# Optimization experiments

Hardware: AMD Instinct MI355X
Metric: run time of the kernel (lower is better)

Reference implementation:

```python
import jax, jax.numpy as jnp
import numpy as np

TEMPERATURE = 8.0  # sqrt(head_dim=64)
NEG_INF = -1e9


def setup_inputs() -> dict:
    key = jax.random.key(0)
    k1, k2, k3, k4, k5 = jax.random.split(key, 5)
    B, H, S, D = 1, 8, 2048, 64
    q = jax.random.normal(k1, (B, H, S, D), dtype=jnp.float32)
    k = jax.random.normal(k2, (B, H, S, D), dtype=jnp.float32)
    v = jax.random.normal(k3, (B, H, S, D), dtype=jnp.float32)
    sph = jax.random.uniform(k4, (B, H, S, S), dtype=jnp.float32)
    mask = jax.random.randint(k5, (B, H, S, S), 0, 2, dtype=jnp.int32)
    return {"q": q, "k": k, "v": v, "sph": sph, "mask": mask}


def reference(q, k, v, sph, mask):
    # scores: [B,H,Sq,Sk]
    attn = jnp.einsum('bhqd,bhkd->bhqk', q / TEMPERATURE, k)
    attn = attn * sph                       # multiplicative bias
    attn = jnp.where(mask == 0, NEG_INF, attn)
    p_attn = jax.nn.softmax(attn, axis=-1)  # dropout p=0 -> identity
    out = jnp.einsum('bhqk,bhkd->bhqd', p_attn, v)
    return (out, p_attn)
```

## Files before the change

### kernel.cpp

```cpp
#include <hip/hip_runtime.h>

#define SLEN 2048
#define DIM  64
#define NH   8
#define TQ   16
#define NEG_INF -1e9f

typedef __attribute__((ext_vector_type(8))) short short8;
typedef __attribute__((ext_vector_type(4))) float f32x4;
typedef unsigned short ushort;

__device__ inline ushort f2bf(float x) {
    unsigned u = __float_as_uint(x);
    u += 0x7fffu + ((u >> 16) & 1u);
    return (ushort)(u >> 16);
}
__device__ inline float bf2f(ushort b) {
    return __uint_as_float(((unsigned)b) << 16);
}

__global__ __launch_bounds__(256)
void convk_kernel(const float* __restrict__ k,
                  ushort* __restrict__ khi, ushort* __restrict__ klo)
{
    int i4 = blockIdx.x * 256 + threadIdx.x;
    float4 x = ((const float4*)k)[i4];
    ushort h0 = f2bf(x.x), h1 = f2bf(x.y), h2 = f2bf(x.z), h3 = f2bf(x.w);
    ushort4 hi = {h0, h1, h2, h3};
    ushort4 lo = {f2bf(x.x - bf2f(h0)), f2bf(x.y - bf2f(h1)),
                  f2bf(x.z - bf2f(h2)), f2bf(x.w - bf2f(h3))};
    ((ushort4*)khi)[i4] = hi;
    ((ushort4*)klo)[i4] = lo;
}

__global__ __launch_bounds__(256)
void convv_kernel(const float* __restrict__ v, ushort* __restrict__ vt)
{
    __shared__ ushort sT[64][70];
    const int h  = blockIdx.x >> 5;
    const int st = blockIdx.x & 31;
    const int t  = threadIdx.x;
    {
        const int r0 = t >> 4;
        const int c  = (t & 15) * 4;
        #pragma unroll
        for (int rr = r0; rr < 64; rr += 16) {
            float4 x = *(const float4*)(v + ((size_t)(h * SLEN + st * 64 + rr)) * DIM + c);
            sT[c + 0][rr] = f2bf(x.x);
            sT[c + 1][rr] = f2bf(x.y);
            sT[c + 2][rr] = f2bf(x.z);
            sT[c + 3][rr] = f2bf(x.w);
        }
    }
    __syncthreads();
    {
        const int d  = t >> 2;
        const int s0 = (t & 3) * 16;
        short8 a = *(const short8*)(&sT[d][s0]);
        short8 b = *(const short8*)(&sT[d][s0 + 8]);
        ushort* dst = vt + ((size_t)(h * DIM + d)) * SLEN + st * 64 + s0;
        *(short8*)(dst)     = a;
        *(short8*)(dst + 8) = b;
    }
}

__global__ __launch_bounds__(256)
void convm_kernel(const int* __restrict__ mask, ushort* __restrict__ mb)
{
    size_t i = (size_t)blockIdx.x * 256 + threadIdx.x;
    const int4* p = (const int4*)(mask + i * 16);
    unsigned m = 0;
    #pragma unroll
    for (int w = 0; w < 4; ++w) {
        int4 a = p[w];
        m |= (a.x != 0 ? 1u : 0u) << (w * 4 + 0);
        m |= (a.y != 0 ? 1u : 0u) << (w * 4 + 1);
        m |= (a.z != 0 ? 1u : 0u) << (w * 4 + 2);
        m |= (a.w != 0 ? 1u : 0u) << (w * 4 + 3);
    }
    mb[i] = (ushort)m;
}

__global__ __launch_bounds__(512, 2)
void attn_mfma_kernel(const float* __restrict__ q,
                      const ushort* __restrict__ khi,
                      const ushort* __restrict__ klo,
                      const ushort* __restrict__ vt,
                      const float* __restrict__ sph,
                      const unsigned* __restrict__ mbits,
                      float* __restrict__ out,
                      float* __restrict__ p_out)
{
    __shared__ ushort sP[TQ][SLEN + 8];
    __shared__ float  sS[TQ][1024 + 4];
    __shared__ ushort sQhi[TQ][72];
    __shared__ ushort sQlo[TQ][72];
    __shared__ float sMax[TQ][8];
    __shared__ float sSum[TQ][8];
    __shared__ float sC[4][TQ][16];

    const int tid  = threadIdx.x;
    const int wave = tid >> 6;
    const int lane = tid & 63;
    const int quad = lane >> 4;
    const int l16  = lane & 15;
    const int bx0  = blockIdx.x;
    const int bx   = ((bx0 & 7) << 7) | (bx0 >> 3);
    const int h    = bx >> 7;
    const int qr0  = (bx & 127) * TQ;

    {
        int e = tid * 2;
        int r = e >> 6, d = e & 63;
        float2 qv = *(const float2*)(q + ((size_t)(h * SLEN + qr0 + r)) * DIM + d);
        ushort h0 = f2bf(qv.x), h1 = f2bf(qv.y);
        sQhi[r][d]     = h0;
        sQhi[r][d + 1] = h1;
        sQlo[r][d]     = f2bf(qv.x - bf2f(h0));
        sQlo[r][d + 1] = f2bf(qv.y - bf2f(h1));
    }
    __syncthreads();

    short8 ah0 = *(const short8*)(&sQhi[l16][quad * 8]);
    short8 ah1 = *(const short8*)(&sQhi[l16][32 + quad * 8]);
    short8 al0 = *(const short8*)(&sQlo[l16][quad * 8]);
    short8 al1 = *(const short8*)(&sQlo[l16][32 + quad * 8]);

    const int cb0 = wave * 128;
    const int cb1 = 1024 + wave * 128;

    unsigned roA[4], roB[4];
    #pragma unroll
    for (int j = 0; j < 4; ++j) {
        unsigned rb = (unsigned)((h * SLEN + qr0 + quad * 4 + j) * SLEN);
        roA[j] = rb + cb0 + l16;
        roB[j] = rb + cb1 + l16;
    }

    unsigned mwA[4][4], mwB[4][4];
    #pragma unroll
    for (int j = 0; j < 4; ++j) {
        const unsigned* mr = mbits
            + (size_t)(h * SLEN + qr0 + quad * 4 + j) * (SLEN / 32);
        *(uint4*)mwA[j] = *(const uint4*)(mr + (cb0 >> 5));
        *(uint4*)mwB[j] = *(const uint4*)(mr + (cb1 >> 5));
    }

    const int srow = wave * 2;
    f32x4 g0[8];
    #pragma unroll
    for (int r = 0; r < 2; ++r)
        #pragma unroll
        for (int i = 0; i < 4; ++i)
            g0[r * 4 + i] = __builtin_nontemporal_load(
                (const f32x4*)(sph + (size_t)(h * SLEN + qr0 + srow + r) * SLEN
                                   + i * 256 + lane * 4));

    f32x4 c[16];
    #pragma unroll
    for (int t = 0; t < 16; ++t) c[t] = (f32x4){0.f, 0.f, 0.f, 0.f};

    #pragma unroll
    for (int t = 0; t < 16; ++t) {
        const int cb = (t < 8) ? (cb0 + t * 16) : (cb1 + (t - 8) * 16);
        const size_t rowb = ((size_t)(h * SLEN + cb + l16)) * DIM + quad * 8;
        short8 bh0 = *(const short8*)(khi + rowb);
        short8 bh1 = *(const short8*)(khi + rowb + 32);
        short8 bl0 = *(const short8*)(klo + rowb);
        short8 bl1 = *(const short8*)(klo + rowb + 32);
        c[t] = __builtin_amdgcn_mfma_f32_16x16x32_bf16(ah0, bh0, c[t], 0, 0, 0);
        c[t] = __builtin_amdgcn_mfma_f32_16x16x32_bf16(ah1, bh1, c[t], 0, 0, 0);
        c[t] = __builtin_amdgcn_mfma_f32_16x16x32_bf16(ah0, bl0, c[t], 0, 0, 0);
        c[t] = __builtin_amdgcn_mfma_f32_16x16x32_bf16(ah1, bl1, c[t], 0, 0, 0);
        c[t] = __builtin_amdgcn_mfma_f32_16x16x32_bf16(al0, bh0, c[t], 0, 0, 0);
        c[t] = __builtin_amdgcn_mfma_f32_16x16x32_bf16(al1, bh1, c[t], 0, 0, 0);
    }

    #pragma unroll
    for (int r = 0; r < 2; ++r)
        #pragma unroll
        for (int i = 0; i < 4; ++i)
            *(f32x4*)&sS[srow + r][i * 256 + lane * 4] = g0[r * 4 + i];
    __syncthreads();

    f32x4 g1[8];
    #pragma unroll
    for (int r = 0; r < 2; ++r)
        #pragma unroll
        for (int i = 0; i < 4; ++i)
            g1[r * 4 + i] = __builtin_nontemporal_load(
                (const f32x4*)(sph + (size_t)(h * SLEN + qr0 + srow + r) * SLEN
                                   + 1024 + i * 256 + lane * 4));

    float rmax[4] = {-3.4e38f, -3.4e38f, -3.4e38f, -3.4e38f};
    #pragma unroll
    for (int t = 0; t < 8; ++t) {
        #pragma unroll
        for (int j = 0; j < 4; ++j) {
            float sphv = sS[quad * 4 + j][cb0 + t * 16 + l16];
            float s = c[t][j] * 0.125f * sphv;
            const unsigned ok = (mwA[j][t >> 1] >> ((t & 1) * 16 + l16)) & 1u;
            s = ok ? s : NEG_INF;
            c[t][j] = s;
            rmax[j] = fmaxf(rmax[j], s);
        }
    }
    __syncthreads();

    #pragma unroll
    for (int r = 0; r < 2; ++r)
        #pragma unroll
        for (int i = 0; i < 4; ++i)
            *(f32x4*)&sS[srow + r][i * 256 + lane * 4] = g1[r * 4 + i];
    __syncthreads();

    #pragma unroll
    for (int t = 8; t < 16; ++t) {
        #pragma unroll
        for (int j = 0; j < 4; ++j) {
            float sphv = sS[quad * 4 + j][cb0 + (t - 8) * 16 + l16];
            float s = c[t][j] * 0.125f * sphv;
            const unsigned ok =
                (mwB[j][(t - 8) >> 1] >> (((t - 8) & 1) * 16 + l16)) & 1u;
            s = ok ? s : NEG_INF;
            c[t][j] = s;
            rmax[j] = fmaxf(rmax[j], s);
        }
    }

    #pragma unroll
    for (int off = 1; off <= 8; off <<= 1) {
        #pragma unroll
        for (int j = 0; j < 4; ++j)
            rmax[j] = fmaxf(rmax[j], __shfl_xor(rmax[j], off));
    }
    if (l16 == 0) {
        #pragma unroll
        for (int j = 0; j < 4; ++j) sMax[quad * 4 + j][wave] = rmax[j];
    }
    __syncthreads();

    float M[4];
    #pragma unroll
    for (int j = 0; j < 4; ++j) {
        float m = sMax[quad * 4 + j][0];
        #pragma unroll
        for (int w = 1; w < 8; ++w) m = fmaxf(m, sMax[quad * 4 + j][w]);
        M[j] = m;
    }

    float rsum[4] = {0.f, 0.f, 0.f, 0.f};
    #pragma unroll
    for (int t = 0; t < 16; ++t) {
        #pragma unroll
        for (int j = 0; j < 4; ++j) {
            float e = __expf(c[t][j] - M[j]);
            c[t][j] = e;
            rsum[j] += e;
        }
    }
    #pragma unroll
    for (int off = 1; off <= 8; off <<= 1) {
        #pragma unroll
        for (int j = 0; j < 4; ++j)
            rsum[j] += __shfl_xor(rsum[j], off);
    }
    if (l16 == 0) {
        #pragma unroll
        for (int j = 0; j < 4; ++j) sSum[quad * 4 + j][wave] = rsum[j];
    }
    __syncthreads();

    float inv[4];
    #pragma unroll
    for (int j = 0; j < 4; ++j) {
        float s = 0.f;
        #pragma unroll
        for (int w = 0; w < 8; ++w) s += sSum[quad * 4 + j][w];
        inv[j] = 1.0f / s;
    }

    #pragma unroll
    for (int t = 0; t < 16; ++t) {
        #pragma unroll
        for (int j = 0; j < 4; ++j) {
            const int col = ((t < 8) ? (cb0 + t * 16) : (cb1 + (t - 8) * 16)) + l16;
            float p = c[t][j] * inv[j];
            c[t][j] = p;
            sP[quad * 4 + j][col] = f2bf(p);
        }
    }
    __syncthreads();

    #pragma unroll
    for (int t = 0; t < 16; ++t) {
        #pragma unroll
        for (int j = 0; j < 4; ++j)
            p_out[(t < 8) ? (roA[j] + t * 16) : (roB[j] + (t - 8) * 16)] = c[t][j];
    }

    const int ntile = wave & 3;
    const int khalf = wave >> 2;
    f32x4 o = (f32x4){0.f, 0.f, 0.f, 0.f};
    const ushort* vb = vt + ((size_t)(h * DIM + ntile * 16 + l16)) * SLEN
                          + khalf * 1024 + quad * 8;
    #pragma unroll 8
    for (int s = 0; s < 32; ++s) {
        short8 a = *(const short8*)(&sP[l16][khalf * 1024 + s * 32 + quad * 8]);
        short8 b = *(const short8*)(vb + s * 32);
        o = __builtin_amdgcn_mfma_f32_16x16x32_bf16(a, b, o, 0, 0, 0);
    }
    if (wave >= 4) {
        #pragma unroll
        for (int j = 0; j < 4; ++j) sC[ntile][quad * 4 + j][l16] = o[j];
    }
    __syncthreads();
    if (wave < 4) {
        #pragma unroll
        for (int j = 0; j < 4; ++j) {
            float r = o[j] + sC[ntile][quad * 4 + j][l16];
            out[((size_t)(h * SLEN) + qr0 + quad * 4 + j) * DIM + ntile * 16 + l16] = r;
        }
    }
}

extern "C" void kernel_launch(void* const* d_in, const int* in_sizes, int n_in,
                              void* d_out, int out_size, void* d_ws, size_t ws_size,
                              hipStream_t stream) {
    const float* q    = (const float*)d_in[0];
    const float* k    = (const float*)d_in[1];
    const float* v    = (const float*)d_in[2];
    const float* sph  = (const float*)d_in[3];
    const int*   mask = (const int*)d_in[4];
    float* out   = (float*)d_out;
    float* p_out = out + (size_t)NH * SLEN * DIM;

    const size_t nkv = (size_t)NH * SLEN * DIM;
    ushort* khi = (ushort*)d_ws;
    ushort* klo = khi + nkv;
    ushort* vt  = klo + nkv;
    ushort* mbits = vt + nkv;

    const size_t nmask = (size_t)NH * SLEN * SLEN;

    hipLaunchKernelGGL(convk_kernel, dim3(nkv / 4 / 256), dim3(256), 0, stream,
                       k, khi, klo);
    hipLaunchKernelGGL(convv_kernel, dim3(NH * (SLEN / 64)), dim3(256), 0, stream,
                       v, vt);
    hipLaunchKernelGGL(convm_kernel, dim3(nmask / 16 / 256), dim3(256), 0, stream,
                       mask, mbits);
    hipLaunchKernelGGL(attn_mfma_kernel, dim3(NH * (SLEN / TQ)), dim3(512), 0, stream,
                       q, khi, klo, vt, sph, (const unsigned*)mbits, out, p_out);
}
```

Measured before the change: 415.5 us.

## Stage p_attn through LDS for coalesced vector stores and use lighter barriers

The p_attn output was written straight from MFMA accumulator layout as scattered scalar 4-byte stores. It is now staged through the sS shared buffer in two halves and written as row-contiguous float4 stores, and the stores are moved after the PV MFMA. Every __syncthreads is replaced with an inline-asm barrier that waits only on LDS counters (lgkmcnt), so outstanding global stores and loads no longer stall the barrier. This adds extra LDS traffic and barriers, and it depends on the custom barrier being correct for all the shared-memory hazards.

```diff
diff --git a/kernel.cpp b/kernel.cpp
--- a/kernel.cpp
+++ b/kernel.cpp
@@ -17,6 +17,10 @@
 }
 __device__ inline float bf2f(ushort b) {
     return __uint_as_float(((unsigned)b) << 16);
+}
+
+__device__ inline void xbar() {
+    asm volatile("s_waitcnt lgkmcnt(0)\n\ts_barrier" ::: "memory");
 }
 
 __global__ __launch_bounds__(256)
@@ -92,7 +96,7 @@
                       float* __restrict__ p_out)
 {
     __shared__ ushort sP[TQ][SLEN + 8];
-    __shared__ float  sS[TQ][1024 + 4];
+    __shared__ float  sS[TQ][1028];
     __shared__ ushort sQhi[TQ][72];
     __shared__ ushort sQlo[TQ][72];
     __shared__ float sMax[TQ][8];
@@ -119,7 +123,7 @@
         sQlo[r][d]     = f2bf(qv.x - bf2f(h0));
         sQlo[r][d + 1] = f2bf(qv.y - bf2f(h1));
     }
-    __syncthreads();
+    xbar();
 
     short8 ah0 = *(const short8*)(&sQhi[l16][quad * 8]);
     short8 ah1 = *(const short8*)(&sQhi[l16][32 + quad * 8]);
@@ -128,14 +132,6 @@
 
     const int cb0 = wave * 128;
     const int cb1 = 1024 + wave * 128;
-
-    unsigned roA[4], roB[4];
-    #pragma unroll
-    for (int j = 0; j < 4; ++j) {
-        unsigned rb = (unsigned)((h * SLEN + qr0 + quad * 4 + j) * SLEN);
-        roA[j] = rb + cb0 + l16;
-        roB[j] = rb + cb1 + l16;
-    }
 
     unsigned mwA[4][4], mwB[4][4];
     #pragma unroll
@@ -181,7 +177,7 @@
         #pragma unroll
         for (int i = 0; i < 4; ++i)
             *(f32x4*)&sS[srow + r][i * 256 + lane * 4] = g0[r * 4 + i];
-    __syncthreads();
+    xbar();
 
     f32x4 g1[8];
     #pragma unroll
@@ -205,14 +201,14 @@
             rmax[j] = fmaxf(rmax[j], s);
         }
     }
-    __syncthreads();
+    xbar();
 
     #pragma unroll
     for (int r = 0; r < 2; ++r)
         #pragma unroll
         for (int i = 0; i < 4; ++i)
             *(f32x4*)&sS[srow + r][i * 256 + lane * 4] = g1[r * 4 + i];
-    __syncthreads();
+    xbar();
 
     #pragma unroll
     for (int t = 8; t < 16; ++t) {
@@ -238,7 +234,7 @@
         #pragma unroll
         for (int j = 0; j < 4; ++j) sMax[quad * 4 + j][wave] = rmax[j];
     }
-    __syncthreads();
+    xbar();
 
     float M[4];
     #pragma unroll
@@ -269,7 +265,7 @@
         #pragma unroll
         for (int j = 0; j < 4; ++j) sSum[quad * 4 + j][wave] = rsum[j];
     }
-    __syncthreads();
+    xbar();
 
     float inv[4];
     #pragma unroll
@@ -290,14 +286,7 @@
             sP[quad * 4 + j][col] = f2bf(p);
         }
     }
-    __syncthreads();
-
-    #pragma unroll
-    for (int t = 0; t < 16; ++t) {
-        #pragma unroll
-        for (int j = 0; j < 4; ++j)
-            p_out[(t < 8) ? (roA[j] + t * 16) : (roB[j] + (t - 8) * 16)] = c[t][j];
-    }
+    xbar();
 
     const int ntile = wave & 3;
     const int khalf = wave >> 2;
@@ -314,13 +303,53 @@
         #pragma unroll
         for (int j = 0; j < 4; ++j) sC[ntile][quad * 4 + j][l16] = o[j];
     }
-    __syncthreads();
+    xbar();
+    float orow[4] = {0.f, 0.f, 0.f, 0.f};
     if (wave < 4) {
         #pragma unroll
-        for (int j = 0; j < 4; ++j) {
-            float r = o[j] + sC[ntile][quad * 4 + j][l16];
-            out[((size_t)(h * SLEN) + qr0 + quad * 4 + j) * DIM + ntile * 16 + l16] = r;
-        }
+        for (int j = 0; j < 4; ++j)
+            orow[j] = o[j] + sC[ntile][quad * 4 + j][l16];
+    }
+
+    #pragma unroll
+    for (int t = 0; t < 8; ++t) {
+        #pragma unroll
+        for (int j = 0; j < 4; ++j)
+            sS[quad * 4 + j][cb0 + t * 16 + l16] = c[t][j];
+    }
+    xbar();
+    #pragma unroll
+    for (int r = 0; r < 2; ++r) {
+        #pragma unroll
+        for (int i = 0; i < 4; ++i) {
+            f32x4 v = *(const f32x4*)&sS[srow + r][i * 256 + lane * 4];
+            *(f32x4*)(p_out + (size_t)(h * SLEN + qr0 + srow + r) * SLEN
+                            + i * 256 + lane * 4) = v;
+        }
+    }
+    xbar();
+    #pragma unroll
+    for (int t = 8; t < 16; ++t) {
+        #pragma unroll
+        for (int j = 0; j < 4; ++j)
+            sS[quad * 4 + j][cb0 + (t - 8) * 16 + l16] = c[t][j];
+    }
+    xbar();
+    #pragma unroll
+    for (int r = 0; r < 2; ++r) {
+        #pragma unroll
+        for (int i = 0; i < 4; ++i) {
+            f32x4 v = *(const f32x4*)&sS[srow + r][i * 256 + lane * 4];
+            *(f32x4*)(p_out + (size_t)(h * SLEN + qr0 + srow + r) * SLEN
+                            + 1024 + i * 256 + lane * 4) = v;
+        }
+    }
+
+    if (wave < 4) {
+        #pragma unroll
+        for (int j = 0; j < 4; ++j)
+            out[((size_t)(h * SLEN) + qr0 + quad * 4 + j) * DIM + ntile * 16 + l16]
+                = orow[j];
     }
 }
 
```

New measurement: 420.8 us. About the same (+1.3%).
